# Kernel tuning notes

Measured on AMD Instinct MI355X. Metric: run time of the kernel, lower is better.

Reference implementation:

```python
import jax, jax.numpy as jnp
import numpy as np

DIM, H, M = 1024, 8, 512
DH = DIM // H


def setup_inputs() -> dict:
    key = jax.random.key(0)
    k1, k2 = jax.random.split(key)
    z = jax.random.normal(k1, (8, 4096, DIM), dtype=jnp.float32)
    codebook = jax.random.normal(k2, (H, M, DH), dtype=jnp.float32) * 0.02
    return {"z": z, "codebook": codebook}


def reference(z, codebook):
    """Hard straight-through multi-head VQ quantisation.

    z:        [B, L, dim]
    codebook: [H, M, d_head]
    Returns (z_q [B,L,dim], indices [B,L,H], per_head_distances [B,L,H]).
    """
    B, L, _ = z.shape
    z_h = z.reshape(B, L, H, DH)                       # [B,L,H,dh]
    # squared-L2 distances, batched over all heads at once
    z_sq = jnp.sum(z_h * z_h, axis=-1, keepdims=True)  # [B,L,H,1]
    c_sq = jnp.sum(codebook * codebook, axis=-1)       # [H,M]
    cross = jnp.einsum('blhd,hmd->blhm', z_h, codebook)
    dists = jnp.maximum(z_sq + c_sq[None, None] - 2.0 * cross, 0.0)  # [B,L,H,M]
    idx = jnp.argmin(dists, axis=-1)                   # [B,L,H]
    min_d = jnp.take_along_axis(dists, idx[..., None], axis=-1)[..., 0]  # [B,L,H]
    # gather nearest codebook entry per head: codebook[h, idx[b,l,h]]
    e = codebook[jnp.arange(H)[None, None, :], idx]    # [B,L,H,dh]
    # straight-through: forward value = e, gradient = identity to z
    z_q_h = z_h + jax.lax.stop_gradient(e - z_h)
    z_q = z_q_h.reshape(B, L, DIM)
    return z_q, idx, min_d
```

## Files before the change

### kernel.cpp

```cpp
#include <hip/hip_runtime.h>
#include <cfloat>
#include <cstdint>

#define H_    8
#define DH_   128
#define M_    512
#define DIM_  1024
#define BL_   32768

#define BPOS    128
#define THREADS 512
#define NC      128
#define NCHUNK  (M_ / NC)
#define CAP     16
#define EPS     0.02f

typedef _Float16 half8 __attribute__((ext_vector_type(8)));
typedef float floatx4 __attribute__((ext_vector_type(4)));

#define WS_CB_BYTES (H_ * M_ * DH_ * 2)
#define WS_CSQ_OFF  WS_CB_BYTES

#define OFF_CB   0
#define OFF_ZSQ  (OFF_CB + 32768)
#define OFF_CNT  (OFF_ZSQ + 512)
#define OFF_CI   (OFF_CNT + 512)
#define OFF_WIN  (OFF_CI + 8192)
#define LDS_TOTAL (OFF_WIN + 512)

extern __shared__ char smem[];

__device__ __forceinline__ int swz(int row, int g) { return (g ^ (row & 15)) << 4; }

__device__ __forceinline__ half8 cvt8(float4 a, float4 b) {
    half8 h;
    h[0]=(_Float16)a.x; h[1]=(_Float16)a.y; h[2]=(_Float16)a.z; h[3]=(_Float16)a.w;
    h[4]=(_Float16)b.x; h[5]=(_Float16)b.y; h[6]=(_Float16)b.z; h[7]=(_Float16)b.w;
    return h;
}

__device__ __forceinline__ float exact_d(const float* __restrict__ zr,
                                         const float* __restrict__ cr,
                                         float zsq)
{
    float cx0=0,cx1=0,cx2=0,cx3=0,cq0=0,cq1=0,cq2=0,cq3=0;
    #pragma unroll 8
    for (int k4 = 0; k4 < 32; ++k4) {
        float4 a = *(const float4*)(zr + k4 * 4);
        float4 b = *(const float4*)(cr + k4 * 4);
        cx0 = fmaf(a.x, b.x, cx0); cx1 = fmaf(a.y, b.y, cx1);
        cx2 = fmaf(a.z, b.z, cx2); cx3 = fmaf(a.w, b.w, cx3);
        cq0 = fmaf(b.x, b.x, cq0); cq1 = fmaf(b.y, b.y, cq1);
        cq2 = fmaf(b.z, b.z, cq2); cq3 = fmaf(b.w, b.w, cq3);
    }
    float cross = (cx0 + cx1) + (cx2 + cx3);
    float csqe  = (cq0 + cq1) + (cq2 + cq3);
    float d = (zsq + csqe) - 2.0f * cross;
    return fmaxf(d, 0.f);
}

__global__ __launch_bounds__(256) void prep_kernel(const float* __restrict__ cbk,
                                                   half8* __restrict__ cbw,
                                                   float* __restrict__ csqw)
{
    int t = blockIdx.x * 256 + threadIdx.x;
    int g = t & 15;
    int row = t >> 4;
    int gs = g ^ (row & 15);
    const float* src = cbk + (size_t)row * DH_ + gs * 8;
    float4 v0 = *(const float4*)src;
    float4 v1 = *(const float4*)(src + 4);
    cbw[row * 16 + g] = cvt8(v0, v1);

    if (g == 0) {
        const float* cr = cbk + (size_t)row * DH_;
        float ax=0.f, ay=0.f, az=0.f, aw=0.f;
        #pragma unroll
        for (int c4 = 0; c4 < 32; ++c4) {
            float4 v = *(const float4*)(cr + c4 * 4);
            ax = fmaf(v.x, v.x, ax); ay = fmaf(v.y, v.y, ay);
            az = fmaf(v.z, v.z, az); aw = fmaf(v.w, v.w, aw);
        }
        csqw[row] = (ax + ay) + (az + aw);
    }
}

__global__ __launch_bounds__(THREADS, 6) void vq_kernel(
    const float* __restrict__ z,
    const float* __restrict__ cbk,
    const char*  __restrict__ cbw,
    const float* __restrict__ csqw,
    float* __restrict__ out_zq,
    float* __restrict__ out_idx,
    float* __restrict__ out_mind)
{
    char*  cbB  = smem + OFF_CB;
    float* zsqS = (float*)(smem + OFF_ZSQ);
    int*   cntS = (int*)(smem + OFF_CNT);
    int*   candI = (int*)(smem + OFF_CI);
    int*   winS  = (int*)(smem + OFF_WIN);

    const int tid   = threadIdx.x;
    const int lane  = tid & 63;
    const int w     = tid >> 6;
    const int bx    = blockIdx.x;
    const int h     = bx & 7;
    const int posBase = (bx >> 3) * BPOS;

    const float* zBlk = z   + (size_t)posBase * DIM_ + h * DH_;
    const float* cbH  = cbk + (size_t)h * M_ * DH_;
    const char*  cbWH = cbw + (size_t)h * M_ * 256;
    const float* csqH = csqw + h * M_;

    if (tid < BPOS) cntS[tid] = 0;

    if (tid < BPOS) {
        const float* zr = zBlk + (size_t)tid * DIM_;
        float ax=0.f, ay=0.f, az=0.f, aw=0.f;
        #pragma unroll
        for (int c4 = 0; c4 < 32; ++c4) {
            float4 v = *(const float4*)(zr + c4 * 4);
            ax = fmaf(v.x, v.x, ax); ay = fmaf(v.y, v.y, ay);
            az = fmaf(v.z, v.z, az); aw = fmaf(v.w, v.w, aw);
        }
        zsqS[tid] = (ax + ay) + (az + aw);
    }

    half8 afr[4];
    {
        int row = (w << 4) + (lane & 15);
        const float* zr = zBlk + (size_t)row * DIM_;
        #pragma unroll
        for (int ks = 0; ks < 4; ++ks) {
            int g = ks * 4 + (lane >> 4);
            float4 v0 = *(const float4*)(zr + g * 8);
            float4 v1 = *(const float4*)(zr + g * 8 + 4);
            afr[ks] = cvt8(v0, v1);
        }
    }

    float rmin[4] = {FLT_MAX, FLT_MAX, FLT_MAX, FLT_MAX};

    #pragma unroll
    for (int ch = 0; ch < NCHUNK; ++ch) {
        const int mBase = ch * NC;

        {
            const char* src = cbWH + (size_t)mBase * 256;
            #pragma unroll
            for (int it = 0; it < 4; ++it) {
                int off = (tid + THREADS * it) * 16;
                __builtin_amdgcn_global_load_lds(
                    (const __attribute__((address_space(1))) unsigned int*)(src + off),
                    (__attribute__((address_space(3))) unsigned int*)(cbB + off),
                    16, 0, 0);
            }
        }
        __syncthreads();

        floatx4 acc[8];
        #pragma unroll
        for (int nt = 0; nt < 8; ++nt) acc[nt] = (floatx4){0.f, 0.f, 0.f, 0.f};

        #pragma unroll
        for (int ks = 0; ks < 4; ++ks) {
            int g = ks * 4 + (lane >> 4);
            half8 bn[8];
            #pragma unroll
            for (int nt = 0; nt < 8; ++nt) {
                int crow = nt * 16 + (lane & 15);
                bn[nt] = *(const half8*)(cbB + crow * 256 + swz(crow, g));
            }
            #pragma unroll
            for (int nt = 0; nt < 8; ++nt)
                acc[nt] = __builtin_amdgcn_mfma_f32_16x16x32_f16(afr[ks], bn[nt], acc[nt], 0, 0, 0);
        }

        float cs[8];
        #pragma unroll
        for (int nt = 0; nt < 8; ++nt) cs[nt] = csqH[mBase + nt * 16 + (lane & 15)];
        const int colm = mBase + (lane & 15);

        #pragma unroll
        for (int r = 0; r < 4; ++r) {
            float v[8];
            #pragma unroll
            for (int nt = 0; nt < 8; ++nt) v[nt] = fmaf(-2.f, acc[nt][r], cs[nt]);
            float pm = fminf(fminf(fminf(v[0], v[1]), fminf(v[2], v[3])),
                             fminf(fminf(v[4], v[5]), fminf(v[6], v[7])));
            pm = fminf(pm, __shfl_xor(pm, 1, 16));
            pm = fminf(pm, __shfl_xor(pm, 2, 16));
            pm = fminf(pm, __shfl_xor(pm, 4, 16));
            pm = fminf(pm, __shfl_xor(pm, 8, 16));
            rmin[r] = fminf(rmin[r], pm);
            float thr = rmin[r] + EPS;
            int row = (w << 4) + (lane >> 4) * 4 + r;
            #pragma unroll
            for (int nt = 0; nt < 8; ++nt) {
                if (v[nt] <= thr) {
                    int slot = atomicAdd(&cntS[row], 1);
                    if (slot < CAP) candI[row * CAP + slot] = colm + nt * 16;
                }
            }
        }
        __syncthreads();
    }

    {
        int row = tid >> 2, j = tid & 3;
        int cnt = cntS[row];
        float zsq = zsqS[row];
        const float* zr = zBlk + (size_t)row * DIM_;

        float bd = FLT_MAX; int bi = 0x7fffffff;
        if (cnt > CAP) {
            for (int m = j; m < M_; m += 4) {
                float d = exact_d(zr, cbH + (size_t)m * DH_, zsq);
                if (d < bd || (d == bd && m < bi)) { bd = d; bi = m; }
            }
        } else {
            for (int c = j; c < cnt; c += 4) {
                int m = candI[row * CAP + c];
                float d = exact_d(zr, cbH + (size_t)m * DH_, zsq);
                if (d < bd || (d == bd && m < bi)) { bd = d; bi = m; }
            }
        }
        #pragma unroll
        for (int off = 1; off < 4; off <<= 1) {
            float od = __shfl_xor(bd, off, 4);
            int   oi = __shfl_xor(bi, off, 4);
            if (od < bd || (od == bd && oi < bi)) { bd = od; bi = oi; }
        }
        if (j == 0) {
            if (bi < 0 || bi >= M_) bi = 0;
            size_t gp = (size_t)(posBase + row) * H_ + h;
            out_idx[gp]  = (float)bi;
            out_mind[gp] = bd;
            winS[row] = bi;
        }
    }
    __syncthreads();

    #pragma unroll
    for (int it = 0; it < 8; ++it) {
        int gidx = tid + THREADS * it;
        int row = gidx >> 5, c4 = gidx & 31;
        int m = winS[row];
        float4 v = *(const float4*)(cbH + (size_t)m * DH_ + c4 * 4);
        *(float4*)(out_zq + (size_t)(posBase + row) * DIM_ + h * DH_ + c4 * 4) = v;
    }
}

extern "C" void kernel_launch(void* const* d_in, const int* in_sizes, int n_in,
                              void* d_out, int out_size, void* d_ws, size_t ws_size,
                              hipStream_t stream) {
    const float* z   = (const float*)d_in[0];
    const float* cbk = (const float*)d_in[1];

    float* zq    = (float*)d_out;
    float* oidx  = zq + (size_t)BL_ * DIM_;
    float* omind = oidx + (size_t)BL_ * H_;

    half8* cbw  = (half8*)d_ws;
    float* csqw = (float*)((char*)d_ws + WS_CSQ_OFF);

    hipLaunchKernelGGL(prep_kernel, dim3(256), dim3(256), 0, stream,
                       cbk, cbw, csqw);

    dim3 grid((BL_ / BPOS) * H_);
    dim3 block(THREADS);
    hipLaunchKernelGGL(vq_kernel, grid, block, LDS_TOTAL, stream,
                       z, cbk, (const char*)cbw, csqw, zq, oidx, omind);
}
```

Baseline: 190.9 us.

## Double-buffer codebook chunks in LDS and stage fp16 z tile through shared memory

```diff
diff --git a/kernel.cpp b/kernel.cpp
--- a/kernel.cpp
+++ b/kernel.cpp
@@ -10,8 +10,9 @@
 
 #define BPOS    128
 #define THREADS 512
-#define NC      128
+#define NC      64
 #define NCHUNK  (M_ / NC)
+#define CBUF    16384
 #define CAP     16
 #define EPS     0.02f
 
@@ -21,7 +22,8 @@
 #define WS_CB_BYTES (H_ * M_ * DH_ * 2)
 #define WS_CSQ_OFF  WS_CB_BYTES
 
-#define OFF_CB   0
+#define OFF_Z16  0
+#define OFF_CB   (OFF_Z16 + 32768)
 #define OFF_ZSQ  (OFF_CB + 32768)
 #define OFF_CNT  (OFF_ZSQ + 512)
 #define OFF_CI   (OFF_CNT + 512)
@@ -85,7 +87,7 @@
     }
 }
 
-__global__ __launch_bounds__(THREADS, 6) void vq_kernel(
+__global__ __launch_bounds__(THREADS, 4) void vq_kernel(
     const float* __restrict__ z,
     const float* __restrict__ cbk,
     const char*  __restrict__ cbw,
@@ -94,6 +96,7 @@
     float* __restrict__ out_idx,
     float* __restrict__ out_mind)
 {
+    char*  z16  = smem + OFF_Z16;
     char*  cbB  = smem + OFF_CB;
     float* zsqS = (float*)(smem + OFF_ZSQ);
     int*   cntS = (int*)(smem + OFF_CNT);
@@ -114,6 +117,30 @@
 
     if (tid < BPOS) cntS[tid] = 0;
 
+    {
+        const char* src = cbWH;
+        #pragma unroll
+        for (int it = 0; it < 2; ++it) {
+            int off = tid * 16 + it * 8192;
+            __builtin_amdgcn_global_load_lds(
+                (const __attribute__((address_space(1))) unsigned int*)(src + off),
+                (__attribute__((address_space(3))) unsigned int*)(cbB + off),
+                16, 0, 0);
+        }
+    }
+
+    {
+        int row = tid >> 2, j = tid & 3;
+        const float* zr = zBlk + (size_t)row * DIM_;
+        #pragma unroll
+        for (int k = 0; k < 4; ++k) {
+            int g = j + 4 * k;
+            float4 v0 = *(const float4*)(zr + g * 8);
+            float4 v1 = *(const float4*)(zr + g * 8 + 4);
+            *(half8*)(z16 + row * 256 + swz(row, g)) = cvt8(v0, v1);
+        }
+    }
+
     if (tid < BPOS) {
         const float* zr = zBlk + (size_t)tid * DIM_;
         float ax=0.f, ay=0.f, az=0.f, aw=0.f;
@@ -125,69 +152,66 @@
         }
         zsqS[tid] = (ax + ay) + (az + aw);
     }
+    __syncthreads();
 
     half8 afr[4];
     {
         int row = (w << 4) + (lane & 15);
-        const float* zr = zBlk + (size_t)row * DIM_;
-        #pragma unroll
-        for (int ks = 0; ks < 4; ++ks) {
-            int g = ks * 4 + (lane >> 4);
-            float4 v0 = *(const float4*)(zr + g * 8);
-            float4 v1 = *(const float4*)(zr + g * 8 + 4);
-            afr[ks] = cvt8(v0, v1);
-        }
+        #pragma unroll
+        for (int ks = 0; ks < 4; ++ks)
+            afr[ks] = *(const half8*)(z16 + row * 256 + swz(row, ks * 4 + (lane >> 4)));
     }
 
     float rmin[4] = {FLT_MAX, FLT_MAX, FLT_MAX, FLT_MAX};
+    int cur = 0;
 
     #pragma unroll
     for (int ch = 0; ch < NCHUNK; ++ch) {
         const int mBase = ch * NC;
 
-        {
-            const char* src = cbWH + (size_t)mBase * 256;
-            #pragma unroll
-            for (int it = 0; it < 4; ++it) {
-                int off = (tid + THREADS * it) * 16;
+        if (ch < NCHUNK - 1) {
+            const char* src = cbWH + (size_t)(mBase + NC) * 256;
+            char* dst = cbB + (cur ^ 1) * CBUF;
+            #pragma unroll
+            for (int it = 0; it < 2; ++it) {
+                int off = tid * 16 + it * 8192;
                 __builtin_amdgcn_global_load_lds(
                     (const __attribute__((address_space(1))) unsigned int*)(src + off),
-                    (__attribute__((address_space(3))) unsigned int*)(cbB + off),
+                    (__attribute__((address_space(3))) unsigned int*)(dst + off),
                     16, 0, 0);
             }
         }
-        __syncthreads();
-
-        floatx4 acc[8];
-        #pragma unroll
-        for (int nt = 0; nt < 8; ++nt) acc[nt] = (floatx4){0.f, 0.f, 0.f, 0.f};
+
+        const char* cb = cbB + cur * CBUF;
+        floatx4 acc[4];
+        #pragma unroll
+        for (int nt = 0; nt < 4; ++nt) acc[nt] = (floatx4){0.f, 0.f, 0.f, 0.f};
 
         #pragma unroll
         for (int ks = 0; ks < 4; ++ks) {
             int g = ks * 4 + (lane >> 4);
-            half8 bn[8];
-            #pragma unroll
-            for (int nt = 0; nt < 8; ++nt) {
+            half8 bn[4];
+            #pragma unroll
+            for (int nt = 0; nt < 4; ++nt) {
                 int crow = nt * 16 + (lane & 15);
-                bn[nt] = *(const half8*)(cbB + crow * 256 + swz(crow, g));
-            }
-            #pragma unroll
-            for (int nt = 0; nt < 8; ++nt)
+                bn[nt] = *(const half8*)(cb + crow * 256 + swz(crow, g));
+            }
+            #pragma unroll
+            for (int nt = 0; nt < 4; ++nt)
                 acc[nt] = __builtin_amdgcn_mfma_f32_16x16x32_f16(afr[ks], bn[nt], acc[nt], 0, 0, 0);
         }
 
-        float cs[8];
-        #pragma unroll
-        for (int nt = 0; nt < 8; ++nt) cs[nt] = csqH[mBase + nt * 16 + (lane & 15)];
+        float cs[4];
+        #pragma unroll
+        for (int nt = 0; nt < 4; ++nt) cs[nt] = csqH[mBase + nt * 16 + (lane & 15)];
         const int colm = mBase + (lane & 15);
 
         #pragma unroll
         for (int r = 0; r < 4; ++r) {
-            float v[8];
-            #pragma unroll
-            for (int nt = 0; nt < 8; ++nt) v[nt] = fmaf(-2.f, acc[nt][r], cs[nt]);
-            float pm = fminf(fminf(fminf(v[0], v[1]), fminf(v[2], v[3])),
-                             fminf(fminf(v[4], v[5]), fminf(v[6], v[7])));
+            float v[4];
+            #pragma unroll
+            for (int nt = 0; nt < 4; ++nt) v[nt] = fmaf(-2.f, acc[nt][r], cs[nt]);
+            float pm = fminf(fminf(v[0], v[1]), fminf(v[2], v[3]));
             pm = fminf(pm, __shfl_xor(pm, 1, 16));
             pm = fminf(pm, __shfl_xor(pm, 2, 16));
             pm = fminf(pm, __shfl_xor(pm, 4, 16));
@@ -196,7 +220,7 @@
             float thr = rmin[r] + EPS;
             int row = (w << 4) + (lane >> 4) * 4 + r;
             #pragma unroll
-            for (int nt = 0; nt < 8; ++nt) {
+            for (int nt = 0; nt < 4; ++nt) {
                 if (v[nt] <= thr) {
                     int slot = atomicAdd(&cntS[row], 1);
                     if (slot < CAP) candI[row * CAP + slot] = colm + nt * 16;
@@ -204,6 +228,7 @@
             }
         }
         __syncthreads();
+        cur ^= 1;
     }
 
     {
@@ -267,6 +292,9 @@
     hipLaunchKernelGGL(prep_kernel, dim3(256), dim3(256), 0, stream,
                        cbk, cbw, csqw);
 
+    hipFuncSetAttribute((const void*)vq_kernel,
+                        hipFuncAttributeMaxDynamicSharedMemorySize, LDS_TOTAL);
+
     dim3 grid((BL_ / BPOS) * H_);
     dim3 block(THREADS);
     hipLaunchKernelGGL(vq_kernel, grid, block, LDS_TOTAL, stream,
```

After: 193.4 us. About the same (+1.3%).

## Stage z fp16 tile and codebook norms in LDS, reorder chunk loads

Applied to the files above, without the earlier changes.

```diff
diff --git a/kernel.cpp b/kernel.cpp
--- a/kernel.cpp
+++ b/kernel.cpp
@@ -21,9 +21,11 @@
 #define WS_CB_BYTES (H_ * M_ * DH_ * 2)
 #define WS_CSQ_OFF  WS_CB_BYTES
 
-#define OFF_CB   0
+#define OFF_Z16  0
+#define OFF_CB   (OFF_Z16 + 32768)
 #define OFF_ZSQ  (OFF_CB + 32768)
-#define OFF_CNT  (OFF_ZSQ + 512)
+#define OFF_CSQ  (OFF_ZSQ + 512)
+#define OFF_CNT  (OFF_CSQ + 512)
 #define OFF_CI   (OFF_CNT + 512)
 #define OFF_WIN  (OFF_CI + 8192)
 #define LDS_TOTAL (OFF_WIN + 512)
@@ -85,7 +87,7 @@
     }
 }
 
-__global__ __launch_bounds__(THREADS, 6) void vq_kernel(
+__global__ __launch_bounds__(THREADS, 4) void vq_kernel(
     const float* __restrict__ z,
     const float* __restrict__ cbk,
     const char*  __restrict__ cbw,
@@ -94,8 +96,10 @@
     float* __restrict__ out_idx,
     float* __restrict__ out_mind)
 {
+    char*  z16  = smem + OFF_Z16;
     char*  cbB  = smem + OFF_CB;
     float* zsqS = (float*)(smem + OFF_ZSQ);
+    float* csqS = (float*)(smem + OFF_CSQ);
     int*   cntS = (int*)(smem + OFF_CNT);
     int*   candI = (int*)(smem + OFF_CI);
     int*   winS  = (int*)(smem + OFF_WIN);
@@ -110,33 +114,48 @@
     const float* zBlk = z   + (size_t)posBase * DIM_ + h * DH_;
     const float* cbH  = cbk + (size_t)h * M_ * DH_;
     const char*  cbWH = cbw + (size_t)h * M_ * 256;
-    const float* csqH = csqw + h * M_;
-
+    const float* csqHw = csqw + h * M_;
+
+    #pragma unroll
+    for (int it = 0; it < 4; ++it) {
+        int off = tid * 16 + it * 8192;
+        __builtin_amdgcn_global_load_lds(
+            (const __attribute__((address_space(1))) unsigned int*)(cbWH + off),
+            (__attribute__((address_space(3))) unsigned int*)(cbB + off),
+            16, 0, 0);
+    }
+    if (tid < 32) {
+        int off = tid * 16;
+        __builtin_amdgcn_global_load_lds(
+            (const __attribute__((address_space(1))) unsigned int*)((const char*)csqHw + off),
+            (__attribute__((address_space(3))) unsigned int*)((char*)csqS + off),
+            16, 0, 0);
+    }
     if (tid < BPOS) cntS[tid] = 0;
 
     if (tid < BPOS) {
         const float* zr = zBlk + (size_t)tid * DIM_;
         float ax=0.f, ay=0.f, az=0.f, aw=0.f;
         #pragma unroll
-        for (int c4 = 0; c4 < 32; ++c4) {
-            float4 v = *(const float4*)(zr + c4 * 4);
-            ax = fmaf(v.x, v.x, ax); ay = fmaf(v.y, v.y, ay);
-            az = fmaf(v.z, v.z, az); aw = fmaf(v.w, v.w, aw);
+        for (int k = 0; k < 16; ++k) {
+            float4 v0 = *(const float4*)(zr + k * 8);
+            float4 v1 = *(const float4*)(zr + k * 8 + 4);
+            ax = fmaf(v0.x, v0.x, ax); ay = fmaf(v0.y, v0.y, ay);
+            az = fmaf(v0.z, v0.z, az); aw = fmaf(v0.w, v0.w, aw);
+            ax = fmaf(v1.x, v1.x, ax); ay = fmaf(v1.y, v1.y, ay);
+            az = fmaf(v1.z, v1.z, az); aw = fmaf(v1.w, v1.w, aw);
+            *(half8*)(z16 + tid * 256 + swz(tid, k)) = cvt8(v0, v1);
         }
         zsqS[tid] = (ax + ay) + (az + aw);
     }
+    __syncthreads();
 
     half8 afr[4];
     {
         int row = (w << 4) + (lane & 15);
-        const float* zr = zBlk + (size_t)row * DIM_;
-        #pragma unroll
-        for (int ks = 0; ks < 4; ++ks) {
-            int g = ks * 4 + (lane >> 4);
-            float4 v0 = *(const float4*)(zr + g * 8);
-            float4 v1 = *(const float4*)(zr + g * 8 + 4);
-            afr[ks] = cvt8(v0, v1);
-        }
+        #pragma unroll
+        for (int ks = 0; ks < 4; ++ks)
+            afr[ks] = *(const half8*)(z16 + row * 256 + swz(row, ks * 4 + (lane >> 4)));
     }
 
     float rmin[4] = {FLT_MAX, FLT_MAX, FLT_MAX, FLT_MAX};
@@ -145,19 +164,6 @@
     for (int ch = 0; ch < NCHUNK; ++ch) {
         const int mBase = ch * NC;
 
-        {
-            const char* src = cbWH + (size_t)mBase * 256;
-            #pragma unroll
-            for (int it = 0; it < 4; ++it) {
-                int off = (tid + THREADS * it) * 16;
-                __builtin_amdgcn_global_load_lds(
-                    (const __attribute__((address_space(1))) unsigned int*)(src + off),
-                    (__attribute__((address_space(3))) unsigned int*)(cbB + off),
-                    16, 0, 0);
-            }
-        }
-        __syncthreads();
-
         floatx4 acc[8];
         #pragma unroll
         for (int nt = 0; nt < 8; ++nt) acc[nt] = (floatx4){0.f, 0.f, 0.f, 0.f};
@@ -178,7 +184,7 @@
 
         float cs[8];
         #pragma unroll
-        for (int nt = 0; nt < 8; ++nt) cs[nt] = csqH[mBase + nt * 16 + (lane & 15)];
+        for (int nt = 0; nt < 8; ++nt) cs[nt] = csqS[nt * 16 + (lane & 15)];
         const int colm = mBase + (lane & 15);
 
         #pragma unroll
@@ -203,8 +209,29 @@
                 }
             }
         }
-        __syncthreads();
-    }
+
+        if (ch < NCHUNK - 1) {
+            __syncthreads();
+            const char* src = cbWH + (size_t)(mBase + NC) * 256;
+            #pragma unroll
+            for (int it = 0; it < 4; ++it) {
+                int off = tid * 16 + it * 8192;
+                __builtin_amdgcn_global_load_lds(
+                    (const __attribute__((address_space(1))) unsigned int*)(src + off),
+                    (__attribute__((address_space(3))) unsigned int*)(cbB + off),
+                    16, 0, 0);
+            }
+            if (tid < 32) {
+                int off = tid * 16;
+                __builtin_amdgcn_global_load_lds(
+                    (const __attribute__((address_space(1))) unsigned int*)((const char*)csqHw + (mBase + NC) * 4 + off),
+                    (__attribute__((address_space(3))) unsigned int*)((char*)csqS + off),
+                    16, 0, 0);
+            }
+            __syncthreads();
+        }
+    }
+    __syncthreads();
 
     {
         int row = tid >> 2, j = tid & 3;
@@ -267,6 +294,9 @@
     hipLaunchKernelGGL(prep_kernel, dim3(256), dim3(256), 0, stream,
                        cbk, cbw, csqw);
 
+    hipFuncSetAttribute((const void*)vq_kernel,
+                        hipFuncAttributeMaxDynamicSharedMemorySize, LDS_TOTAL);
+
     dim3 grid((BL_ / BPOS) * H_);
     dim3 block(THREADS);
     hipLaunchKernelGGL(vq_kernel, grid, block, LDS_TOTAL, stream,
```

New measurement: 154.3 us. -19.2%, faster.
